# Performance work log

Hardware: AMD Instinct MI355X
Metric: run time of the kernel (lower is better)

## Reference

```python
import jax, jax.numpy as jnp
import numpy as np
import math

D_MODEL, N_HEADS, D_FF = 512, 8, 2048
B, S = 2, 2048
EPS = 1e-6


def _layernorm(x, g, b):
    mu = jnp.mean(x, axis=-1, keepdims=True)
    var = jnp.mean((x - mu) ** 2, axis=-1, keepdims=True)
    return (x - mu) * jax.lax.rsqrt(var + EPS) * g + b


def setup_inputs() -> dict:
    key = jax.random.key(0)
    ks = jax.random.split(key, 16)
    sd = 1.0 / math.sqrt(D_MODEL)
    return {
        "x": jax.random.normal(ks[0], (B, S, D_MODEL), jnp.float32),
        "sensor_weights": jax.random.uniform(ks[1], (B, S, 4), jnp.float32),
        "mask": jnp.ones((1, 1, S, S), jnp.int32),
        "Wq": jax.random.normal(ks[2], (D_MODEL, D_MODEL), jnp.float32) * sd,
        "Wk": jax.random.normal(ks[3], (D_MODEL, D_MODEL), jnp.float32) * sd,
        "Wv": jax.random.normal(ks[4], (D_MODEL, D_MODEL), jnp.float32) * sd,
        "Wo": jax.random.normal(ks[5], (D_MODEL, D_MODEL), jnp.float32) * sd,
        "bo": jnp.zeros((D_MODEL,), jnp.float32),
        "sensor_attention": jnp.ones((N_HEADS, 4), jnp.float32),  # init = ones
        "temporal_bias": jax.random.normal(ks[6], (1, N_HEADS, 1, 1), jnp.float32) * 0.02,
        "ln1_g": jnp.ones((D_MODEL,), jnp.float32),
        "ln1_b": jnp.zeros((D_MODEL,), jnp.float32),
        "ln2_g": jnp.ones((D_MODEL,), jnp.float32),
        "ln2_b": jnp.zeros((D_MODEL,), jnp.float32),
        "W1": jax.random.normal(ks[7], (D_MODEL, D_FF), jnp.float32) * sd,
        "b1": jnp.zeros((D_FF,), jnp.float32),
        "W2": jax.random.normal(ks[8], (D_FF, D_MODEL), jnp.float32) * (1.0 / math.sqrt(D_FF)),
        "b2": jnp.zeros((D_MODEL,), jnp.float32),
    }


def reference(x, sensor_weights, mask, Wq, Wk, Wv, Wo, bo, sensor_attention,
              temporal_bias, ln1_g, ln1_b, ln2_g, ln2_b, W1, b1, W2, b2):
    b, s, d = x.shape
    h = temporal_bias.shape[1]
    dk = d // h
    scale = math.sqrt(dk)

    # [b, h, s, dk]
    q = (x @ Wq).reshape(b, s, h, dk).transpose(0, 2, 1, 3)
    k = (x @ Wk).reshape(b, s, h, dk).transpose(0, 2, 1, 3)
    v = (x @ Wv).reshape(b, s, h, dk).transpose(0, 2, 1, 3)

    scores = jnp.einsum('bhqd,bhkd->bhqk', q, k) / scale  # [b,h,s,s]
    scores = scores + temporal_bias
    # sensor bias: [h,4] x [b,s,4] -> [b,h,s], added per query row
    sensor_bias = jnp.einsum('hf,bsf->bhs', sensor_attention, sensor_weights)
    scores = scores + sensor_bias[..., None]
    scores = jnp.where(mask == 0, jnp.asarray(-1e9, scores.dtype), scores)

    attn = jax.nn.softmax(scores, axis=-1)
    ctx = jnp.einsum('bhqk,bhkd->bhqd', attn, v)
    ctx = ctx.transpose(0, 2, 1, 3).reshape(b, s, d)
    attn_out = ctx @ Wo + bo

    x1 = _layernorm(x + attn_out, ln1_g, ln1_b)
    ff = jax.nn.gelu(x1 @ W1 + b1, approximate=False) @ W2 + b2
    x2 = _layernorm(x1 + ff, ln2_g, ln2_b)
    return x2, attn
```

## Files before the change

### kernel.cpp

```cpp
#include <hip/hip_runtime.h>
#include <cstdint>
#include <cstddef>

#define S_LEN 2048
#define DM 512
#define NH 8
#define DK 64
#define DFF 2048
#define BATCH 2
#define NROWS (BATCH*S_LEN)
#define BHN (BATCH*NH)

#define MASKED_L2 (-1.4426950408889634e9f)
#define QSCALE 0.18033688011112042f

typedef __attribute__((ext_vector_type(8))) _Float16 f16x8;
typedef __attribute__((ext_vector_type(4))) _Float16 f16x4;
typedef __attribute__((ext_vector_type(4))) float f32x4;

#define MFMA(a,b,c)   __builtin_amdgcn_mfma_f32_16x16x32_f16(a,b,c,0,0,0)
#define MFMA16(a,b,c) __builtin_amdgcn_mfma_f32_16x16x16f16(a,b,c,0,0,0)

__device__ __forceinline__ unsigned short f2h(float x){
  union{ _Float16 h; unsigned short u; } c; c.h = (_Float16)x; return c.u;
}
__device__ __forceinline__ int sw64(int r, int c){
  return r*64 + ((((c>>3) ^ r) & 7)<<3) + (c&7);
}
__device__ __forceinline__ int sw32(int r, int c){
  return r*32 + ((((c>>3) ^ r) & 3)<<3) + (c&7);
}

__global__ __launch_bounds__(256) void prep_kernel(
    const float* __restrict__ x, const int* __restrict__ mask,
    const float* __restrict__ Wq, const float* __restrict__ Wk,
    const float* __restrict__ Wv, const float* __restrict__ Wo,
    const float* __restrict__ W1, const float* __restrict__ W2,
    unsigned short* __restrict__ xb,
    unsigned short* __restrict__ wqT, unsigned short* __restrict__ wkT,
    unsigned short* __restrict__ wvT, unsigned short* __restrict__ woT,
    unsigned short* __restrict__ w1T, unsigned short* __restrict__ w2T,
    unsigned* __restrict__ maskw)
{
  const int z = blockIdx.y;
  const int t = blockIdx.x;
  const int tid = threadIdx.x;
  if (z < 6){
    const float* W; unsigned short* WT; int K, N;
    switch(z){
      case 0: W=Wq; WT=wqT; K=512;  N=512;  break;
      case 1: W=Wk; WT=wkT; K=512;  N=512;  break;
      case 2: W=Wv; WT=wvT; K=512;  N=512;  break;
      case 3: W=Wo; WT=woT; K=512;  N=512;  break;
      case 4: W=W1; WT=w1T; K=512;  N=2048; break;
      default:W=W2; WT=w2T; K=2048; N=512;  break;
    }
    const int ntiles = N>>5, ktiles = K>>5;
    if (t >= ntiles*ktiles) return;
    const int kt = t / ntiles, nt = t - kt*ntiles;
    __shared__ float tile[32][33];
    const int tx = tid & 31, ty = tid >> 5;
    #pragma unroll
    for (int i=0;i<4;i++){
      int r = ty + i*8;
      tile[r][tx] = W[(size_t)(kt*32 + r)*N + nt*32 + tx];
    }
    __syncthreads();
    #pragma unroll
    for (int i=0;i<4;i++){
      int r = ty + i*8;
      WT[(size_t)(nt*32 + r)*K + kt*32 + tx] = f2h(tile[tx][r]);
    }
  } else if (z == 6){
    size_t base = (size_t)t*2048 + (size_t)tid*8;
    float4 a = *(const float4*)(x + base);
    float4 b = *(const float4*)(x + base + 4);
    union{ unsigned short h[8]; uint4 v; } pk;
    pk.h[0]=f2h(a.x); pk.h[1]=f2h(a.y); pk.h[2]=f2h(a.z); pk.h[3]=f2h(a.w);
    pk.h[4]=f2h(b.x); pk.h[5]=f2h(b.y); pk.h[6]=f2h(b.z); pk.h[7]=f2h(b.w);
    *(uint4*)(xb + base) = pk.v;
  } else {
    if (t >= 512) return;
    const int gid = t*256 + tid;
    const int row = gid >> 6, w = gid & 63;
    const int4* mp = (const int4*)(mask + (size_t)row*2048 + w*32);
    unsigned word = 0;
    #pragma unroll
    for (int j=0;j<8;j++){
      int4 v = mp[j];
      word |= (unsigned)(v.x!=0) << (j*4+0);
      word |= (unsigned)(v.y!=0) << (j*4+1);
      word |= (unsigned)(v.z!=0) << (j*4+2);
      word |= (unsigned)(v.w!=0) << (j*4+3);
    }
    maskw[gid] = word;
  }
}

template<int KD, int EPI>
__global__ __launch_bounds__(256) void gemm_kernel(
    const unsigned short* __restrict__ A,
    const unsigned short* __restrict__ BT0,
    const unsigned short* __restrict__ BT1,
    const unsigned short* __restrict__ BT2,
    const float* __restrict__ bias,
    const float* __restrict__ resid,
    float* __restrict__ outf,
    unsigned short* __restrict__ ob0,
    unsigned short* __restrict__ ob1,
    unsigned short* __restrict__ ob2)
{
  const unsigned short* BT = BT0;
  unsigned short* outb = ob0;
  float scale = 1.0f;
  bool vtrans = false;
  if (EPI == 0){
    const int z = blockIdx.z;
    if (z == 0) scale = QSCALE;
    else if (z == 1){ BT = BT1; outb = ob1; }
    else            { BT = BT2; outb = ob2; vtrans = true; }
  }
  const int m0 = blockIdx.x*64, n0 = blockIdx.y*64;
  const int tid = threadIdx.x;
  const int wid = tid>>6, l = tid&63, quad = l>>4, lc = l&15;
  const int wm = wid&1, wn = wid>>1;
  __shared__ __align__(16) unsigned short As[2][64*32];
  __shared__ __align__(16) unsigned short Bs[2][64*32];
  const int sr = tid>>2, sc = (tid&3)*8;
  const unsigned short* Ap = A  + (size_t)(m0+sr)*KD + sc;
  const unsigned short* Bp = BT + (size_t)(n0+sr)*KD + sc;
  {
    uint4 va = *(const uint4*)Ap;
    uint4 vb = *(const uint4*)Bp;
    *(uint4*)&As[0][sw32(sr,sc)] = va;
    *(uint4*)&Bs[0][sw32(sr,sc)] = vb;
  }
  f32x4 acc00={0,0,0,0}, acc01={0,0,0,0}, acc10={0,0,0,0}, acc11={0,0,0,0};
  const int ar0 = wm*32 + lc, ar1 = wm*32 + 16 + lc;
  const int br0 = wn*32 + lc, br1 = wn*32 + 16 + lc;
  __syncthreads();
  constexpr int NK = KD/32;
  for (int kk=0; kk<NK; kk++){
    const int cur = kk & 1;
    if (kk+1 < NK){
      uint4 va = *(const uint4*)(Ap + (size_t)(kk+1)*32);
      uint4 vb = *(const uint4*)(Bp + (size_t)(kk+1)*32);
      *(uint4*)&As[cur^1][sw32(sr,sc)] = va;
      *(uint4*)&Bs[cur^1][sw32(sr,sc)] = vb;
    }
    f16x8 a0 = *(const f16x8*)&As[cur][sw32(ar0, quad*8)];
    f16x8 a1 = *(const f16x8*)&As[cur][sw32(ar1, quad*8)];
    f16x8 b0 = *(const f16x8*)&Bs[cur][sw32(br0, quad*8)];
    f16x8 b1 = *(const f16x8*)&Bs[cur][sw32(br1, quad*8)];
    acc00 = MFMA(a0,b0,acc00);
    acc01 = MFMA(a0,b1,acc01);
    acc10 = MFMA(a1,b0,acc10);
    acc11 = MFMA(a1,b1,acc11);
    __syncthreads();
  }
  f32x4 accs[2][2] = {{acc00,acc01},{acc10,acc11}};
  #pragma unroll
  for (int mt=0;mt<2;mt++){
    #pragma unroll
    for (int nt=0;nt<2;nt++){
      f32x4 v = accs[mt][nt];
      const int col  = n0 + wn*32 + nt*16 + lc;
      const int row0 = m0 + wm*32 + mt*16 + quad*4;
      if (EPI == 0 && vtrans){
        const int h = col>>6, d = col&63, b = row0>>11, s0 = row0&2047;
        union{ unsigned short h4[4]; uint2 u; } pk;
        #pragma unroll
        for (int r=0;r<4;r++) pk.h4[r] = f2h(v[r]);
        *(uint2*)(outb + (((size_t)(b*NH + h))*DK + d)*S_LEN + s0) = pk.u;
      } else {
        #pragma unroll
        for (int r=0;r<4;r++){
          const int row = row0 + r;
          const float val = v[r];
          if (EPI == 0){
            const int h = col>>6, d = col&63, b = row>>11, s = row&2047;
            outb[(((size_t)(b*NH + h))*S_LEN + s)*DK + d] = f2h(val*scale);
          } else if (EPI == 1){
            const size_t idx = (size_t)row*DM + col;
            outf[idx] = val + bias[col] + resid[idx];
          } else {
            const float xx = val + bias[col];
            const float gg = 0.5f*xx*(1.0f + erff(xx*0.70710678118654752f));
            outb[(size_t)row*DFF + col] = f2h(gg);
          }
        }
      }
    }
  }
}

__global__ __launch_bounds__(256) void kattn_kernel(
    const unsigned short* __restrict__ qw,
    const unsigned short* __restrict__ kw,
    const unsigned short* __restrict__ vwT,
    const unsigned* __restrict__ maskw,
    float* __restrict__ attn,
    unsigned short* __restrict__ ctx)
{
  const int bh = blockIdx.y, q0 = blockIdx.x*64;
  const int tid = threadIdx.x, wid = tid>>6, l = tid&63, quad = l>>4, lc = l&15;
  __shared__ __align__(16) unsigned short Qs[64*64];
  __shared__ __align__(16) unsigned short Ks[2][64*64];
  __shared__ __align__(16) unsigned short Vs[2][64*64];
  const unsigned short* qbase = qw + ((size_t)bh*S_LEN + q0)*DK;
  const unsigned short* kbase = kw + (size_t)bh*S_LEN*DK;
  const unsigned short* vbase = vwT + (size_t)bh*DK*S_LEN;

  auto stageK = [&](unsigned short* dst, const unsigned short* src){
    #pragma unroll
    for (int i=0;i<2;i++){
      const int idx = tid + i*256, r = idx>>3, c0 = (idx&7)*8;
      *(uint4*)&dst[sw64(r,c0)] = *(const uint4*)(src + (size_t)r*DK + c0);
    }
  };
  auto stageV = [&](unsigned short* dst, const unsigned short* src){
    #pragma unroll
    for (int i=0;i<2;i++){
      const int idx = tid + i*256, d = idx>>3, k0 = (idx&7)*8;
      union { uint4 u; uint2 v2[2]; } U;
      U.u = *(const uint4*)(src + (size_t)d*S_LEN + k0);
      const int g0 = k0>>2;
      *(uint2*)&dst[(g0  )*256 + (((d ^  g0   )&63)<<2)] = U.v2[0];
      *(uint2*)&dst[(g0+1)*256 + (((d ^ (g0+1))&63)<<2)] = U.v2[1];
    }
  };

  #pragma unroll
  for (int i=0;i<2;i++){
    const int idx = tid + i*256, r = idx>>3, c0 = (idx&7)*8;
    *(uint4*)&Qs[sw64(r,c0)] = *(const uint4*)(qbase + (size_t)r*DK + c0);
  }
  stageK(Ks[0], kbase);
  __syncthreads();

  f16x8 bQ0, bQ1;
  {
    const int r = wid*16 + lc;
    bQ0 = *(const f16x8*)&Qs[sw64(r, quad*8)];
    bQ1 = *(const f16x8*)&Qs[sw64(r, 32 + quad*8)];
  }
  const int rowq = q0 + wid*16 + lc;
  const unsigned* mrow = maskw + (size_t)rowq*64;

  float m = -3e38f, ls = 0.f;
  for (int c=0;c<32;c++){
    const int cur = c & 1;
    if (c+1 < 32) stageK(Ks[cur^1], kbase + (size_t)(c+1)*64*DK);
    const uint2 mw = *(const uint2*)(mrow + c*2);
    float sv[4][4];
    __builtin_amdgcn_s_setprio(1);
    #pragma unroll
    for (int nt=0; nt<4; nt++){
      f16x8 aK0 = *(const f16x8*)&Ks[cur][sw64(nt*16+lc, quad*8)];
      f16x8 aK1 = *(const f16x8*)&Ks[cur][sw64(nt*16+lc, 32+quad*8)];
      f32x4 s = {0,0,0,0};
      s = MFMA(aK0, bQ0, s);
      s = MFMA(aK1, bQ1, s);
      const unsigned w = (nt<2) ? mw.x : mw.y;
      #pragma unroll
      for (int r=0;r<4;r++){
        const int sh = (nt&1)*16 + quad*4 + r;
        sv[nt][r] = ((w>>sh)&1u) ? s[r] : MASKED_L2;
      }
    }
    __builtin_amdgcn_s_setprio(0);
    float mc = sv[0][0];
    #pragma unroll
    for (int nt=0;nt<4;nt++)
      #pragma unroll
      for (int r=0;r<4;r++) mc = fmaxf(mc, sv[nt][r]);
    const float m2 = fmaxf(m, mc);
    float add = 0.f;
    #pragma unroll
    for (int nt=0;nt<4;nt++)
      #pragma unroll
      for (int r=0;r<4;r++) add += __builtin_exp2f(sv[nt][r]-m2);
    ls = ls*__builtin_exp2f(m-m2) + add;
    m = m2;
    __syncthreads();
  }
  #pragma unroll
  for (int o=16;o<64;o<<=1){
    const float mo = __shfl_xor(m, o, 64);
    const float lo = __shfl_xor(ls, o, 64);
    const float m2 = fmaxf(m, mo);
    ls = ls*__builtin_exp2f(m-m2) + lo*__builtin_exp2f(mo-m2);
    m = m2;
  }
  const float li = 1.0f/ls;

  stageK(Ks[0], kbase);
  stageV(Vs[0], vbase);
  f32x4 O[4] = {{0,0,0,0},{0,0,0,0},{0,0,0,0},{0,0,0,0}};
  float* arow = attn + (size_t)bh*S_LEN*S_LEN + (size_t)rowq*S_LEN;
  __syncthreads();
  for (int c=0;c<32;c++){
    const int cur = c & 1;
    if (c+1 < 32){
      stageK(Ks[cur^1], kbase + (size_t)(c+1)*64*DK);
      stageV(Vs[cur^1], vbase + (size_t)(c+1)*64);
    }
    const uint2 mw = *(const uint2*)(mrow + c*2);
    __builtin_amdgcn_s_setprio(1);
    #pragma unroll
    for (int nt=0; nt<4; nt++){
      f16x8 aK0 = *(const f16x8*)&Ks[cur][sw64(nt*16+lc, quad*8)];
      f16x8 aK1 = *(const f16x8*)&Ks[cur][sw64(nt*16+lc, 32+quad*8)];
      f32x4 s = {0,0,0,0};
      s = MFMA(aK0, bQ0, s);
      s = MFMA(aK1, bQ1, s);
      const unsigned w = (nt<2) ? mw.x : mw.y;
      f32x4 pv;
      f16x4 bP;
      #pragma unroll
      for (int r=0;r<4;r++){
        const int sh = (nt&1)*16 + quad*4 + r;
        const float se = ((w>>sh)&1u) ? s[r] : MASKED_L2;
        const float p  = __builtin_exp2f(se - m) * li;
        pv[r] = p;
        bP[r] = (_Float16)p;
      }
      __builtin_nontemporal_store(pv, (f32x4*)(arow + (size_t)c*64 + nt*16 + quad*4));
      const int g = nt*4 + quad;
      #pragma unroll
      for (int dt=0; dt<4; dt++){
        f16x4 aV = *(const f16x4*)&Vs[cur][g*256 + ((((dt*16+lc) ^ g)&63)<<2)];
        O[dt] = MFMA16(aV, bP, O[dt]);
      }
    }
    __builtin_amdgcn_s_setprio(0);
    __syncthreads();
  }
  const int b = bh>>3, h = bh&7;
  unsigned short* cb = ctx + ((size_t)b*S_LEN + rowq)*DM + h*DK + quad*4;
  #pragma unroll
  for (int dt=0; dt<4; dt++){
    union{ unsigned short h4[4]; uint2 u; } pk;
    #pragma unroll
    for (int r=0;r<4;r++) pk.h4[r] = f2h(O[dt][r]);
    *(uint2*)(cb + dt*16) = pk.u;
  }
}

__global__ __launch_bounds__(256) void ln_kernel(
    const float* __restrict__ in, const float* __restrict__ g,
    const float* __restrict__ b, float* __restrict__ outf,
    unsigned short* __restrict__ outb)
{
  const int row = blockIdx.x*4 + (threadIdx.x>>6);
  const int l = threadIdx.x & 63;
  const float* p = in + (size_t)row*DM + l*8;
  float4 v0 = *(const float4*)p;
  float4 v1 = *(const float4*)(p+4);
  float vals[8] = {v0.x,v0.y,v0.z,v0.w,v1.x,v1.y,v1.z,v1.w};
  float s = 0.f, q = 0.f;
  #pragma unroll
  for (int j=0;j<8;j++){ s += vals[j]; q += vals[j]*vals[j]; }
  #pragma unroll
  for (int o=1;o<64;o<<=1){ s += __shfl_xor(s,o,64); q += __shfl_xor(q,o,64); }
  const float mu = s*(1.0f/DM);
  const float var = q*(1.0f/DM) - mu*mu;
  const float rs = rsqrtf(var + 1e-6f);
  const float* gp = g + l*8;
  const float* bp = b + l*8;
  float4 g0 = *(const float4*)gp, g1 = *(const float4*)(gp+4);
  float4 bb0 = *(const float4*)bp, bb1 = *(const float4*)(bp+4);
  float gv[8] = {g0.x,g0.y,g0.z,g0.w,g1.x,g1.y,g1.z,g1.w};
  float bv[8] = {bb0.x,bb0.y,bb0.z,bb0.w,bb1.x,bb1.y,bb1.z,bb1.w};
  float ov[8];
  #pragma unroll
  for (int j=0;j<8;j++) ov[j] = (vals[j]-mu)*rs*gv[j] + bv[j];
  float* op = outf + (size_t)row*DM + l*8;
  *(float4*)op     = make_float4(ov[0],ov[1],ov[2],ov[3]);
  *(float4*)(op+4) = make_float4(ov[4],ov[5],ov[6],ov[7]);
  if (outb){
    union{ unsigned short h[8]; uint4 v; } pk;
    #pragma unroll
    for (int j=0;j<8;j++) pk.h[j] = f2h(ov[j]);
    *(uint4*)(outb + (size_t)row*DM + l*8) = pk.v;
  }
}

extern "C" void kernel_launch(void* const* d_in, const int* in_sizes, int n_in,
                              void* d_out, int out_size, void* d_ws, size_t ws_size,
                              hipStream_t stream)
{
  const float* x    = (const float*)d_in[0];
  const int*   mask = (const int*)d_in[2];
  const float* Wq   = (const float*)d_in[3];
  const float* Wk   = (const float*)d_in[4];
  const float* Wv   = (const float*)d_in[5];
  const float* Wo   = (const float*)d_in[6];
  const float* bo   = (const float*)d_in[7];
  const float* ln1g = (const float*)d_in[10];
  const float* ln1b = (const float*)d_in[11];
  const float* ln2g = (const float*)d_in[12];
  const float* ln2b = (const float*)d_in[13];
  const float* W1   = (const float*)d_in[14];
  const float* b1   = (const float*)d_in[15];
  const float* W2   = (const float*)d_in[16];
  const float* b2   = (const float*)d_in[17];

  float* x2_out   = (float*)d_out;
  float* attn_out = x2_out + (size_t)NROWS*DM;

  char* p = (char*)d_ws;
  auto alloc = [&](size_t bytes)->char*{
    char* r = p; p += (bytes + 255) & ~(size_t)255; return r;
  };
  unsigned short* xb   = (unsigned short*)alloc((size_t)NROWS*DM*2);
  unsigned short* wqT  = (unsigned short*)alloc(512*512*2);
  unsigned short* wkT  = (unsigned short*)alloc(512*512*2);
  unsigned short* wvT  = (unsigned short*)alloc(512*512*2);
  unsigned short* woT  = (unsigned short*)alloc(512*512*2);
  unsigned short* w1T  = (unsigned short*)alloc(2048*512*2);
  unsigned short* w2T  = (unsigned short*)alloc(512*2048*2);
  unsigned short* q_ws = (unsigned short*)alloc((size_t)BHN*S_LEN*DK*2);
  unsigned short* k_ws = (unsigned short*)alloc((size_t)BHN*S_LEN*DK*2);
  unsigned short* v_ws = (unsigned short*)alloc((size_t)BHN*S_LEN*DK*2);
  unsigned*       maskw= (unsigned*)alloc((size_t)S_LEN*64*4);
  unsigned short* ctxb = (unsigned short*)alloc((size_t)NROWS*DM*2);
  float*          yv   = (float*)alloc((size_t)NROWS*DM*4);
  float*          x1f  = (float*)alloc((size_t)NROWS*DM*4);
  unsigned short* x1b  = (unsigned short*)alloc((size_t)NROWS*DM*2);
  unsigned short* hb   = (unsigned short*)alloc((size_t)NROWS*DFF*2);
  float*          zv   = (float*)alloc((size_t)NROWS*DM*4);

  prep_kernel<<<dim3(1024,8), 256, 0, stream>>>(
      x, mask, Wq, Wk, Wv, Wo, W1, W2,
      xb, wqT, wkT, wvT, woT, w1T, w2T, maskw);

  gemm_kernel<512,0><<<dim3(64,8,3), 256, 0, stream>>>(
      xb, wqT, wkT, wvT, nullptr, nullptr, nullptr, q_ws, k_ws, v_ws);

  kattn_kernel<<<dim3(32,16), 256, 0, stream>>>(
      q_ws, k_ws, v_ws, maskw, attn_out, ctxb);

  gemm_kernel<512,1><<<dim3(64,8), 256, 0, stream>>>(
      ctxb, woT, nullptr, nullptr, bo, x, yv, nullptr, nullptr, nullptr);

  ln_kernel<<<1024, 256, 0, stream>>>(yv, ln1g, ln1b, x1f, x1b);

  gemm_kernel<512,2><<<dim3(64,32), 256, 0, stream>>>(
      x1b, w1T, nullptr, nullptr, b1, nullptr, nullptr, hb, nullptr, nullptr);

  gemm_kernel<2048,1><<<dim3(64,8), 256, 0, stream>>>(
      hb, w2T, nullptr, nullptr, b2, x1f, zv, nullptr, nullptr, nullptr);

  ln_kernel<<<1024, 256, 0, stream>>>(zv, ln2g, ln2b, x2_out, nullptr);

  (void)in_sizes; (void)n_in; (void)out_size; (void)ws_size;
}
```

Before: 497.9 us.

## Use direct global-to-LDS loads for GEMM and attention K/Q staging

Replaces register-staged global loads followed by LDS stores with global_load_lds direct-to-LDS transfers, using swizzled source addresses so the XOR layout is kept. The GEMM kernel also moves from a 32-wide to a 64-wide K tile, halving the number of loop iterations and barriers at the cost of doubling LDS per buffer. The attention kernel stages Q and K through the same direct path, while V keeps its transposing register path. The aim is to cut VGPR pressure and issue overhead on the load path; correctness depends on the new lane-to-address mapping and on how the barriers wait for these asynchronous loads.

```diff
diff --git a/kernel.cpp b/kernel.cpp
--- a/kernel.cpp
+++ b/kernel.cpp
@@ -27,8 +27,12 @@
 __device__ __forceinline__ int sw64(int r, int c){
   return r*64 + ((((c>>3) ^ r) & 7)<<3) + (c&7);
 }
-__device__ __forceinline__ int sw32(int r, int c){
-  return r*32 + ((((c>>3) ^ r) & 3)<<3) + (c&7);
+
+__device__ __forceinline__ void gld16(void* lds, const void* g){
+  __builtin_amdgcn_global_load_lds(
+      (const __attribute__((address_space(1))) unsigned int*)g,
+      (__attribute__((address_space(3))) unsigned int*)lds,
+      16, 0, 0);
 }
 
 __global__ __launch_bounds__(256) void prep_kernel(
@@ -124,38 +128,44 @@
   const int tid = threadIdx.x;
   const int wid = tid>>6, l = tid&63, quad = l>>4, lc = l&15;
   const int wm = wid&1, wn = wid>>1;
-  __shared__ __align__(16) unsigned short As[2][64*32];
-  __shared__ __align__(16) unsigned short Bs[2][64*32];
-  const int sr = tid>>2, sc = (tid&3)*8;
-  const unsigned short* Ap = A  + (size_t)(m0+sr)*KD + sc;
-  const unsigned short* Bp = BT + (size_t)(n0+sr)*KD + sc;
-  {
-    uint4 va = *(const uint4*)Ap;
-    uint4 vb = *(const uint4*)Bp;
-    *(uint4*)&As[0][sw32(sr,sc)] = va;
-    *(uint4*)&Bs[0][sw32(sr,sc)] = vb;
-  }
+  __shared__ __align__(16) unsigned short As[2][64*64];
+  __shared__ __align__(16) unsigned short Bs[2][64*64];
+  const int lr = l>>3, lg = l&7;
+  const int swcol = ((lg ^ lr) << 3);
+  const unsigned short* Asrc0 = A  + (size_t)(m0 + wid*16 +     lr)*KD + swcol;
+  const unsigned short* Asrc1 = A  + (size_t)(m0 + wid*16 + 8 + lr)*KD + swcol;
+  const unsigned short* Bsrc0 = BT + (size_t)(n0 + wid*16 +     lr)*KD + swcol;
+  const unsigned short* Bsrc1 = BT + (size_t)(n0 + wid*16 + 8 + lr)*KD + swcol;
+  const int cb0 = wid*1024, cb1 = wid*1024 + 512;
+
+  gld16(&As[0][cb0], Asrc0);  gld16(&As[0][cb1], Asrc1);
+  gld16(&Bs[0][cb0], Bsrc0);  gld16(&Bs[0][cb1], Bsrc1);
+
   f32x4 acc00={0,0,0,0}, acc01={0,0,0,0}, acc10={0,0,0,0}, acc11={0,0,0,0};
   const int ar0 = wm*32 + lc, ar1 = wm*32 + 16 + lc;
   const int br0 = wn*32 + lc, br1 = wn*32 + 16 + lc;
   __syncthreads();
-  constexpr int NK = KD/32;
+  constexpr int NK = KD/64;
   for (int kk=0; kk<NK; kk++){
     const int cur = kk & 1;
     if (kk+1 < NK){
-      uint4 va = *(const uint4*)(Ap + (size_t)(kk+1)*32);
-      uint4 vb = *(const uint4*)(Bp + (size_t)(kk+1)*32);
-      *(uint4*)&As[cur^1][sw32(sr,sc)] = va;
-      *(uint4*)&Bs[cur^1][sw32(sr,sc)] = vb;
-    }
-    f16x8 a0 = *(const f16x8*)&As[cur][sw32(ar0, quad*8)];
-    f16x8 a1 = *(const f16x8*)&As[cur][sw32(ar1, quad*8)];
-    f16x8 b0 = *(const f16x8*)&Bs[cur][sw32(br0, quad*8)];
-    f16x8 b1 = *(const f16x8*)&Bs[cur][sw32(br1, quad*8)];
-    acc00 = MFMA(a0,b0,acc00);
-    acc01 = MFMA(a0,b1,acc01);
-    acc10 = MFMA(a1,b0,acc10);
-    acc11 = MFMA(a1,b1,acc11);
+      const size_t off = (size_t)(kk+1)*64;
+      gld16(&As[cur^1][cb0], Asrc0 + off);
+      gld16(&As[cur^1][cb1], Asrc1 + off);
+      gld16(&Bs[cur^1][cb0], Bsrc0 + off);
+      gld16(&Bs[cur^1][cb1], Bsrc1 + off);
+    }
+    #pragma unroll
+    for (int ks=0; ks<2; ks++){
+      f16x8 a0 = *(const f16x8*)&As[cur][sw64(ar0, ks*32 + quad*8)];
+      f16x8 a1 = *(const f16x8*)&As[cur][sw64(ar1, ks*32 + quad*8)];
+      f16x8 b0 = *(const f16x8*)&Bs[cur][sw64(br0, ks*32 + quad*8)];
+      f16x8 b1 = *(const f16x8*)&Bs[cur][sw64(br1, ks*32 + quad*8)];
+      acc00 = MFMA(a0,b0,acc00);
+      acc01 = MFMA(a0,b1,acc01);
+      acc10 = MFMA(a1,b0,acc10);
+      acc11 = MFMA(a1,b1,acc11);
+    }
     __syncthreads();
   }
   f32x4 accs[2][2] = {{acc00,acc01},{acc10,acc11}};
@@ -211,12 +221,12 @@
   const unsigned short* kbase = kw + (size_t)bh*S_LEN*DK;
   const unsigned short* vbase = vwT + (size_t)bh*DK*S_LEN;
 
-  auto stageK = [&](unsigned short* dst, const unsigned short* src){
-    #pragma unroll
-    for (int i=0;i<2;i++){
-      const int idx = tid + i*256, r = idx>>3, c0 = (idx&7)*8;
-      *(uint4*)&dst[sw64(r,c0)] = *(const uint4*)(src + (size_t)r*DK + c0);
-    }
+  const int lanoff = ((l>>3)<<6) + (((l&7) ^ (l>>3))<<3);
+  const int cb0 = wid*1024, cb1 = wid*1024 + 512;
+
+  auto stageKg = [&](unsigned short* dst, const unsigned short* tsrc){
+    gld16(dst + cb0, tsrc + cb0 + lanoff);
+    gld16(dst + cb1, tsrc + cb1 + lanoff);
   };
   auto stageV = [&](unsigned short* dst, const unsigned short* src){
     #pragma unroll
@@ -230,12 +240,8 @@
     }
   };
 
-  #pragma unroll
-  for (int i=0;i<2;i++){
-    const int idx = tid + i*256, r = idx>>3, c0 = (idx&7)*8;
-    *(uint4*)&Qs[sw64(r,c0)] = *(const uint4*)(qbase + (size_t)r*DK + c0);
-  }
-  stageK(Ks[0], kbase);
+  stageKg(Qs, qbase);
+  stageKg(Ks[0], kbase);
   __syncthreads();
 
   f16x8 bQ0, bQ1;
@@ -250,7 +256,7 @@
   float m = -3e38f, ls = 0.f;
   for (int c=0;c<32;c++){
     const int cur = c & 1;
-    if (c+1 < 32) stageK(Ks[cur^1], kbase + (size_t)(c+1)*64*DK);
+    if (c+1 < 32) stageKg(Ks[cur^1], kbase + (size_t)(c+1)*64*DK);
     const uint2 mw = *(const uint2*)(mrow + c*2);
     float sv[4][4];
     __builtin_amdgcn_s_setprio(1);
@@ -294,7 +300,7 @@
   }
   const float li = 1.0f/ls;
 
-  stageK(Ks[0], kbase);
+  stageKg(Ks[0], kbase);
   stageV(Vs[0], vbase);
   f32x4 O[4] = {{0,0,0,0},{0,0,0,0},{0,0,0,0},{0,0,0,0}};
   float* arow = attn + (size_t)bh*S_LEN*S_LEN + (size_t)rowq*S_LEN;
@@ -302,7 +308,7 @@
   for (int c=0;c<32;c++){
     const int cur = c & 1;
     if (c+1 < 32){
-      stageK(Ks[cur^1], kbase + (size_t)(c+1)*64*DK);
+      stageKg(Ks[cur^1], kbase + (size_t)(c+1)*64*DK);
       stageV(Vs[cur^1], vbase + (size_t)(c+1)*64);
     }
     const uint2 mw = *(const uint2*)(mrow + c*2);
```

After: 500.9 us. About the same (+0.6%).
